# Kernel optimization log

Measured on AMD Instinct MI355X. Metric: run time of the kernel, lower is better.

## Reference

```python
import jax, jax.numpy as jnp
import numpy as np

N = 262144            # inflated nodes (atoms + edge-nodes)
E = 4 * 1024 * 1024   # directed edges
D = 8                 # node_feature_dim
TD = 1                # time_dim
H = 32                # hidden_channels
L = 4                 # num_layers
BN_EPS = 1e-5


def setup_inputs() -> dict:
    key = jax.random.key(0)
    ks = jax.random.split(key, 12)
    s = 0.1  # small init scale
    return {
        "x": jax.random.normal(ks[0], (N, D), jnp.float32),
        "t": jax.random.uniform(ks[1], (1,), jnp.float32),
        "edge_index": jax.random.randint(ks[2], (2, E), 0, N, jnp.int32),
        "node_mask": jax.random.randint(ks[3], (N,), 0, 2) > 0,
        "edge_mask": jax.random.randint(ks[4], (N,), 0, 2) > 0,
        "ond": 5,  # original_node_feature_dim
        "oed": 4,  # original_edge_feature_dim
        # GINConv MLP params: layer 0 has in=D+TD, layers 1..3 have in=H
        "W1_first": jax.random.normal(ks[5], (D + TD, H), jnp.float32) * s,
        "b1_first": jnp.zeros((H,), jnp.float32),
        "W2_first": jax.random.normal(ks[6], (H, H), jnp.float32) * s,
        "b2_first": jnp.zeros((H,), jnp.float32),
        "W1_rest": jax.random.normal(ks[7], (L - 1, H, H), jnp.float32) * s,
        "b1_rest": jnp.zeros((L - 1, H), jnp.float32),
        "W2_rest": jax.random.normal(ks[8], (L - 1, H, H), jnp.float32) * s,
        "b2_rest": jnp.zeros((L - 1, H), jnp.float32),
        "eps": jnp.zeros((L,), jnp.float32),           # train_eps=True, init 0
        "bn_gamma": jnp.ones((L, H), jnp.float32),
        "bn_beta": jnp.zeros((L, H), jnp.float32),
        "lin_W": jax.random.normal(ks[9], (L * H, D), jnp.float32) * s,
        "lin_b": jnp.zeros((D,), jnp.float32),
    }


def _gin_forward(x, t, W1_first, b1_first, W2_first, b2_first,
                 W1_rest, b1_rest, W2_rest, b2_rest, eps, bn_gamma, bn_beta,
                 lin_W, lin_b, edge_index, node_mask, edge_mask, ond, oed):
    src = edge_index[0]
    dst = edge_index[1]
    n = x.shape[0]
    # x_in = cat(x, t*ones)
    tcol = jnp.full((n, 1), t[0], x.dtype)
    h = jnp.concatenate([x, tcol], axis=1)  # [N, D+TD]
    xs = []
    for l in range(L):
        # GINConv: (1+eps)*x_i + sum_{j->i} x_j, then 2-layer MLP
        agg = jax.ops.segment_sum(h[src], dst, num_segments=n)  # scatter-add
        z = (1.0 + eps[l]) * h + agg
        W1 = W1_first if l == 0 else W1_rest[l - 1]
        b1 = b1_first if l == 0 else b1_rest[l - 1]
        W2 = W2_first if l == 0 else W2_rest[l - 1]
        b2 = b2_first if l == 0 else b2_rest[l - 1]
        z = jax.nn.relu(z @ W1 + b1) @ W2 + b2  # [N, H]
        # BatchNorm (training-mode batch stats), then ReLU; dropout=eval->id
        mu = jnp.mean(z, axis=0)
        var = jnp.var(z, axis=0)
        z = (z - mu) * jax.lax.rsqrt(var + BN_EPS) * bn_gamma[l] + bn_beta[l]
        h = jax.nn.relu(z)
        xs.append(h)
    # JK 'cat' + final Linear(L*H -> D)
    new_x = jnp.concatenate(xs, axis=1) @ lin_W + lin_b  # [N, D]
    # masked feature write-back: x[mask, 1:dim+1] = new_x[mask, 1:dim+1]
    cols = jnp.arange(x.shape[1])
    ncols = (cols >= 1) & (cols < ond + 1)
    ecols = (cols >= 1) & (cols < oed + 1)
    out = jnp.where(node_mask[:, None] & ncols[None, :], new_x, x)
    out = jnp.where(edge_mask[:, None] & ecols[None, :], new_x, out)
    return out


def reference(x, t, edge_index, node_mask, edge_mask, ond, oed,
              W1_first, b1_first, W2_first, b2_first,
              W1_rest, b1_rest, W2_rest, b2_rest,
              eps, bn_gamma, bn_beta, lin_W, lin_b):
    return _gin_forward(x, t, W1_first, b1_first, W2_first, b2_first,
                        W1_rest, b1_rest, W2_rest, b2_rest,
                        eps, bn_gamma, bn_beta, lin_W, lin_b,
                        edge_index, node_mask, edge_mask, ond, oed)
```

## Files before the change

kernel.cpp:

```cpp
#include <hip/hip_runtime.h>
#include <cstdint>

#define NN 262144
#define EE 4194304
#define CAP 64
#define NB 512
#define BSZ 512
#define NSH 8
#define SCAP 1280
#define EPB 8192
#define SLICES 64

__device__ inline float bf2f(unsigned short u) {
  union { unsigned int i; float f; } v; v.i = ((unsigned int)u) << 16; return v.f;
}
__device__ inline unsigned short f2bf(float f) {
  union { float f; unsigned int i; } v; v.f = f;
  unsigned int r = v.i + 0x7FFF + ((v.i >> 16) & 1);
  return (unsigned short)(r >> 16);
}
__device__ inline float blo(unsigned int u) {
  union { unsigned int i; float f; } v; v.i = u << 16; return v.f;
}
__device__ inline float bhi(unsigned int u) {
  union { unsigned int i; float f; } v; v.i = u & 0xFFFF0000u; return v.f;
}

__global__ void k_curinit(int* __restrict__ cur) {
  int i = blockIdx.x * 256 + threadIdx.x;
  if (i < NSH * NB) cur[i] = i * SCAP;
}

__global__ void __launch_bounds__(256, 1)
k_bin(const int* __restrict__ ei, int* __restrict__ cur, int* __restrict__ pair) {
  __shared__ int hist[NB];
  __shared__ int off[NB];
  __shared__ int gbase[NB];
  __shared__ int psum[256];
  __shared__ int ebuf[EPB];
  const int tid = threadIdx.x, blk = blockIdx.x, sh = blk & (NSH - 1);
  const int* esrc = ei + (size_t)blk * EPB;
  const int* edst = ei + EE + (size_t)blk * EPB;

  for (int k = tid; k < NB; k += 256) hist[k] = 0;
  __syncthreads();
  for (int j = tid; j < EPB / 4; j += 256) {
    int4 d4 = ((const int4*)edst)[j];
    atomicAdd(&hist[d4.x >> 9], 1);
    atomicAdd(&hist[d4.y >> 9], 1);
    atomicAdd(&hist[d4.z >> 9], 1);
    atomicAdd(&hist[d4.w >> 9], 1);
  }
  __syncthreads();
  int a0 = hist[2 * tid], a1 = hist[2 * tid + 1];
  int ps = a0 + a1;
  psum[tid] = ps;
  __syncthreads();
  for (int d = 1; d < 256; d <<= 1) {
    int v = (tid >= d) ? psum[tid - d] : 0;
    __syncthreads();
    psum[tid] += v;
    __syncthreads();
  }
  int excl = psum[tid] - ps;
  off[2 * tid] = excl;
  off[2 * tid + 1] = excl + a0;
  __syncthreads();
  for (int b = tid; b < NB; b += 256) {
    int n = hist[b];
    int ci = sh * NB + b;
    gbase[b] = n ? atomicAdd(&cur[ci], n) : ci * SCAP;
  }
  __syncthreads();
  for (int k = tid; k < NB; k += 256) hist[k] = off[k];
  __syncthreads();
  for (int j = tid; j < EPB / 4; j += 256) {
    int4 s4 = ((const int4*)esrc)[j];
    int4 d4 = ((const int4*)edst)[j];
    int dd[4] = {d4.x, d4.y, d4.z, d4.w};
    int ss[4] = {s4.x, s4.y, s4.z, s4.w};
#pragma unroll
    for (int u = 0; u < 4; ++u) {
      int bin = dd[u] >> 9, dl = dd[u] & (BSZ - 1);
      int p = atomicAdd(&hist[bin], 1);
      ebuf[p] = ss[u] | (dl << 18);
    }
  }
  __syncthreads();
  for (int b = tid; b < NB; b += 256) {
    int st = off[b];
    int n = hist[b] - st;
    int ci = sh * NB + b;
    int gb = gbase[b];
    int lim = ci * SCAP + SCAP;
    if (gb + n > lim) n = (lim > gb) ? (lim - gb) : 0;
    for (int k = 0; k < n; ++k) pair[gb + k] = ebuf[st + k];
  }
}

__global__ void k_expand(const int* __restrict__ cur, const int* __restrict__ pair,
                         int* __restrict__ slot, int* __restrict__ deg) {
  __shared__ int cbin[BSZ];
  int tid = threadIdx.x;
  int bin = blockIdx.x;
  for (int k = tid; k < BSZ; k += 512) cbin[k] = 0;
  __syncthreads();
  for (int s = 0; s < NSH; ++s) {
    int ci = s * NB + bin, base = ci * SCAP;
    int cnt = min(cur[ci] - base, SCAP);
    for (int k = tid; k < cnt; k += 512) {
      int p = pair[base + k];
      int src = p & 0x3FFFF, dl = p >> 18;
      int pos = atomicAdd(&cbin[dl], 1);
      if (pos < CAP)
        slot[((size_t)bin * BSZ + dl) * CAP + pos] = src;
    }
  }
  __syncthreads();
  for (int k = tid; k < BSZ; k += 512) {
    int cnt = min(cbin[k], CAP);
    int cntp = (cnt + 15) & ~15;
    int self = bin * BSZ + k;
    for (int p = cnt; p < cntp; ++p)
      slot[((size_t)bin * BSZ + k) * CAP + p] = self;
    deg[bin * BSZ + k] = cnt;
  }
}

__global__ void k_layer0(const float* __restrict__ x, const float* __restrict__ t,
                         const int* __restrict__ slot, const int* __restrict__ deg,
                         const float* __restrict__ W1, const float* __restrict__ b1,
                         const float* __restrict__ W2, const float* __restrict__ b2,
                         const float* __restrict__ epsv,
                         unsigned short* __restrict__ zb,
                         float* __restrict__ ssum, float* __restrict__ ssq) {
  __shared__ float W1s[9 * 32];
  __shared__ float W2s[32 * 32];
  __shared__ float aggs[8][8];
  __shared__ float ins[8][12];
  __shared__ float z1s[8][36];
  __shared__ float sqs[8][36];
  int tid = threadIdx.x;
  int c = tid & 31, g = tid >> 5;
  size_t i = (size_t)blockIdx.x * 8 + g;

  for (int k = tid; k < 9 * 32 / 4; k += 256) ((float4*)W1s)[k] = ((const float4*)W1)[k];
  for (int k = tid; k < 32 * 32 / 4; k += 256) ((float4*)W2s)[k] = ((const float4*)W2)[k];

  int cnt = deg[i];
  int cntp = (cnt + 15) & ~15;
  const int* sl = slot + i * CAP;
  int sv = sl[c];
  float t0 = t[0];
  float epsl = epsv[0];
  float xself = (c < 8) ? x[i * 8 + c] : 0.f;

  int q = c & 1, e = c >> 1;
  float4 agg4 = {0.f, 0.f, 0.f, 0.f};
  int kmax = min(cntp, 32);
  for (int k = 0; k < kmax; k += 16) {
    int s = __shfl(sv, k + e, 32);
    float4 v = ((const float4*)x)[(size_t)s * 2 + q];
    agg4.x += v.x; agg4.y += v.y; agg4.z += v.z; agg4.w += v.w;
  }
  if (cntp > 32) {
    int sv2 = sl[32 + c];
    for (int k = 32; k < cntp; k += 16) {
      int s = __shfl(sv2, (k - 32) + e, 32);
      float4 v = ((const float4*)x)[(size_t)s * 2 + q];
      agg4.x += v.x; agg4.y += v.y; agg4.z += v.z; agg4.w += v.w;
    }
  }
#pragma unroll
  for (int off = 2; off < 32; off <<= 1) {
    agg4.x += __shfl_xor(agg4.x, off, 32);
    agg4.y += __shfl_xor(agg4.y, off, 32);
    agg4.z += __shfl_xor(agg4.z, off, 32);
    agg4.w += __shfl_xor(agg4.w, off, 32);
  }
  if (c < 2) ((float4*)aggs[g])[q] = agg4;
  __syncthreads();

  float pad = (float)(cntp - cnt);
  if (c < 8)       ins[g][c] = (1.f + epsl) * xself + aggs[g][c] - pad * xself;
  else if (c == 8) ins[g][8] = (1.f + epsl) * t0 + (float)cnt * t0;
  __syncthreads();

  float acc = b1[c];
#pragma unroll
  for (int d = 0; d < 9; ++d) acc += ins[g][d] * W1s[d * 32 + c];
  float z1 = fmaxf(acc, 0.f);
  z1s[g][c] = z1;
  __syncthreads();

  float acc2 = b2[c];
#pragma unroll
  for (int d = 0; d < 32; ++d) acc2 += z1s[g][d] * W2s[d * 32 + c];
  zb[i * 32 + c] = f2bf(acc2);

  __syncthreads();
  z1s[g][c] = acc2;
  sqs[g][c] = acc2 * acc2;
  __syncthreads();
  if (g == 0) {
    float s1 = 0.f, s2 = 0.f;
#pragma unroll
    for (int n = 0; n < 8; ++n) { s1 += z1s[n][c]; s2 += sqs[n][c]; }
    int slice = blockIdx.x & (SLICES - 1);
    atomicAdd(&ssum[slice * 32 + c], s1);
    atomicAdd(&ssq[slice * 32 + c], s2);
  }
}

__global__ void k_bnapply(const unsigned short* __restrict__ zb,
                          const float* __restrict__ ssum, const float* __restrict__ ssq,
                          const float* __restrict__ gamma, const float* __restrict__ beta,
                          const float* __restrict__ linW,
                          unsigned short* __restrict__ hb,
                          float* __restrict__ out_acc, int first_acc) {
  __shared__ float linWs[256];
  __shared__ float scs[32], shs[32];
  int tid = threadIdx.x;
  for (int k = tid; k < 256; k += 256) linWs[k] = linW[k];
  if (tid < 32) {
    float s1 = 0.f, s2 = 0.f;
    for (int s = 0; s < SLICES; ++s) { s1 += ssum[s * 32 + tid]; s2 += ssq[s * 32 + tid]; }
    float mu = s1 * (1.f / NN);
    float var = s2 * (1.f / NN) - mu * mu;
    float sc = gamma[tid] * rsqrtf(var + 1e-5f);
    scs[tid] = sc;
    shs[tid] = beta[tid] - mu * sc;
  }
  int r = tid & 3;
  size_t n = (size_t)blockIdx.x * 64 + (tid >> 2);
  uint4 u = ((const uint4*)zb)[n * 4 + r];
  __syncthreads();

  float h[8];
#pragma unroll
  for (int j = 0; j < 8; ++j) {
    unsigned int w = (j < 2) ? u.x : (j < 4) ? u.y : (j < 6) ? u.z : u.w;
    float zv = (j & 1) ? bhi(w) : blo(w);
    h[j] = fmaxf(zv * scs[8 * r + j] + shs[8 * r + j], 0.f);
  }
  uint4 o;
  o.x = (unsigned int)f2bf(h[0]) | ((unsigned int)f2bf(h[1]) << 16);
  o.y = (unsigned int)f2bf(h[2]) | ((unsigned int)f2bf(h[3]) << 16);
  o.z = (unsigned int)f2bf(h[4]) | ((unsigned int)f2bf(h[5]) << 16);
  o.w = (unsigned int)f2bf(h[6]) | ((unsigned int)f2bf(h[7]) << 16);
  ((uint4*)hb)[n * 4 + r] = o;

  float jk[8];
#pragma unroll
  for (int d = 0; d < 8; ++d) {
    float a = 0.f;
#pragma unroll
    for (int j = 0; j < 8; ++j) a += h[j] * linWs[(8 * r + j) * 8 + d];
    jk[d] = a;
  }
#pragma unroll
  for (int off = 1; off <= 2; off <<= 1)
#pragma unroll
    for (int d = 0; d < 8; ++d) jk[d] += __shfl_xor(jk[d], off, 64);
  if (r == 0) {
    float4 a0 = {jk[0], jk[1], jk[2], jk[3]};
    float4 a1 = {jk[4], jk[5], jk[6], jk[7]};
    if (!first_acc) {
      float4 p0 = ((const float4*)out_acc)[n * 2];
      float4 p1 = ((const float4*)out_acc)[n * 2 + 1];
      a0.x += p0.x; a0.y += p0.y; a0.z += p0.z; a0.w += p0.w;
      a1.x += p1.x; a1.y += p1.y; a1.z += p1.z; a1.w += p1.w;
    }
    ((float4*)out_acc)[n * 2] = a0;
    ((float4*)out_acc)[n * 2 + 1] = a1;
  }
}

__global__ void k_layerN(const unsigned short* __restrict__ hb,
                         const int* __restrict__ slot, const int* __restrict__ deg,
                         const float* __restrict__ W1, const float* __restrict__ b1,
                         const float* __restrict__ W2, const float* __restrict__ b2,
                         const float* __restrict__ epsv, int l,
                         unsigned short* __restrict__ zbo,
                         float* __restrict__ ssum, float* __restrict__ ssq) {
  __shared__ float W1s[32 * 32];
  __shared__ float W2s[32 * 32];
  __shared__ float aggs[8][32];
  __shared__ float ins[8][36];
  __shared__ float z1s[8][36];
  int tid = threadIdx.x;
  int c = tid & 31, g = tid >> 5;
  size_t i = (size_t)blockIdx.x * 8 + g;

  for (int k = tid; k < 32 * 32 / 4; k += 256) {
    ((float4*)W1s)[k] = ((const float4*)W1)[k];
    ((float4*)W2s)[k] = ((const float4*)W2)[k];
  }

  float epsl = epsv[l];
  int cnt = deg[i];
  int cntp = (cnt + 15) & ~15;
  const int* sl = slot + i * CAP;
  int sv = sl[c];
  float hself = bf2f(hb[i * 32 + c]);

  int q = c & 7, sub = c >> 3;
  const ushort4* h4 = (const ushort4*)hb;
  float4 agg4 = {0.f, 0.f, 0.f, 0.f};
  int kmax = min(cntp, 32);
  for (int k = 0; k < kmax; k += 16) {
    int sa = __shfl(sv, k + sub, 32);
    int sb = __shfl(sv, k + 4 + sub, 32);
    int sc_ = __shfl(sv, k + 8 + sub, 32);
    int sd = __shfl(sv, k + 12 + sub, 32);
    ushort4 ua = h4[(size_t)sa * 8 + q];
    ushort4 ub = h4[(size_t)sb * 8 + q];
    ushort4 uc = h4[(size_t)sc_ * 8 + q];
    ushort4 ud = h4[(size_t)sd * 8 + q];
    agg4.x += bf2f(ua.x) + bf2f(ub.x) + bf2f(uc.x) + bf2f(ud.x);
    agg4.y += bf2f(ua.y) + bf2f(ub.y) + bf2f(uc.y) + bf2f(ud.y);
    agg4.z += bf2f(ua.z) + bf2f(ub.z) + bf2f(uc.z) + bf2f(ud.z);
    agg4.w += bf2f(ua.w) + bf2f(ub.w) + bf2f(uc.w) + bf2f(ud.w);
  }
  if (cntp > 32) {
    int sv2 = sl[32 + c];
    for (int k = 32; k < cntp; k += 16) {
      int kk = k - 32;
      int sa = __shfl(sv2, kk + sub, 32);
      int sb = __shfl(sv2, kk + 4 + sub, 32);
      int sc_ = __shfl(sv2, kk + 8 + sub, 32);
      int sd = __shfl(sv2, kk + 12 + sub, 32);
      ushort4 ua = h4[(size_t)sa * 8 + q];
      ushort4 ub = h4[(size_t)sb * 8 + q];
      ushort4 uc = h4[(size_t)sc_ * 8 + q];
      ushort4 ud = h4[(size_t)sd * 8 + q];
      agg4.x += bf2f(ua.x) + bf2f(ub.x) + bf2f(uc.x) + bf2f(ud.x);
      agg4.y += bf2f(ua.y) + bf2f(ub.y) + bf2f(uc.y) + bf2f(ud.y);
      agg4.z += bf2f(ua.z) + bf2f(ub.z) + bf2f(uc.z) + bf2f(ud.z);
      agg4.w += bf2f(ua.w) + bf2f(ub.w) + bf2f(uc.w) + bf2f(ud.w);
    }
  }
  agg4.x += __shfl_xor(agg4.x, 8, 32);
  agg4.y += __shfl_xor(agg4.y, 8, 32);
  agg4.z += __shfl_xor(agg4.z, 8, 32);
  agg4.w += __shfl_xor(agg4.w, 8, 32);
  agg4.x += __shfl_xor(agg4.x, 16, 32);
  agg4.y += __shfl_xor(agg4.y, 16, 32);
  agg4.z += __shfl_xor(agg4.z, 16, 32);
  agg4.w += __shfl_xor(agg4.w, 16, 32);
  if (c < 8) ((float4*)aggs[g])[q] = agg4;
  __syncthreads();

  float pad = (float)(cntp - cnt);
  float inval = (1.f + epsl - pad) * hself + aggs[g][c];
  ins[g][c] = inval;
  __syncthreads();

  float acc = b1[c];
#pragma unroll
  for (int d = 0; d < 32; ++d) acc += ins[g][d] * W1s[d * 32 + c];
  float z1 = fmaxf(acc, 0.f);
  z1s[g][c] = z1;
  __syncthreads();

  float acc2 = b2[c];
#pragma unroll
  for (int d = 0; d < 32; ++d) acc2 += z1s[g][d] * W2s[d * 32 + c];
  zbo[i * 32 + c] = f2bf(acc2);

  __syncthreads();
  ins[g][c] = acc2;
  z1s[g][c] = acc2 * acc2;
  __syncthreads();
  if (g == 0) {
    float s1 = 0.f, s2 = 0.f;
#pragma unroll
    for (int n = 0; n < 8; ++n) { s1 += ins[n][c]; s2 += z1s[n][c]; }
    int slice = blockIdx.x & (SLICES - 1);
    atomicAdd(&ssum[slice * 32 + c], s1);
    atomicAdd(&ssq[slice * 32 + c], s2);
  }
}

__global__ void k_final(const unsigned short* __restrict__ z3,
                        const float* __restrict__ ssum, const float* __restrict__ ssq,
                        const float* __restrict__ gamma, const float* __restrict__ beta,
                        const float* __restrict__ linW3, const float* __restrict__ lin_b,
                        const float* __restrict__ out_acc, const float* __restrict__ x,
                        const int* __restrict__ nm, const int* __restrict__ em,
                        const int* __restrict__ ondp, const int* __restrict__ oedp,
                        float* __restrict__ out) {
  __shared__ float linWs[256];
  __shared__ float scs[32], shs[32];
  int tid = threadIdx.x;
  for (int k = tid; k < 256; k += 256) linWs[k] = linW3[k];
  if (tid < 32) {
    float s1 = 0.f, s2 = 0.f;
    for (int s = 0; s < SLICES; ++s) { s1 += ssum[s * 32 + tid]; s2 += ssq[s * 32 + tid]; }
    float mu = s1 * (1.f / NN);
    float var = s2 * (1.f / NN) - mu * mu;
    float sc = gamma[tid] * rsqrtf(var + 1e-5f);
    scs[tid] = sc;
    shs[tid] = beta[tid] - mu * sc;
  }
  int r = tid & 3;
  size_t n = (size_t)blockIdx.x * 64 + (tid >> 2);
  uint4 u = ((const uint4*)z3)[n * 4 + r];
  __syncthreads();

  float h[8];
#pragma unroll
  for (int j = 0; j < 8; ++j) {
    unsigned int w = (j < 2) ? u.x : (j < 4) ? u.y : (j < 6) ? u.z : u.w;
    float zv = (j & 1) ? bhi(w) : blo(w);
    h[j] = fmaxf(zv * scs[8 * r + j] + shs[8 * r + j], 0.f);
  }
  float jk[8];
#pragma unroll
  for (int d = 0; d < 8; ++d) {
    float a = 0.f;
#pragma unroll
    for (int j = 0; j < 8; ++j) a += h[j] * linWs[(8 * r + j) * 8 + d];
    jk[d] = a;
  }
#pragma unroll
  for (int off = 1; off <= 2; off <<= 1)
#pragma unroll
    for (int d = 0; d < 8; ++d) jk[d] += __shfl_xor(jk[d], off, 64);
  if (r == 0) {
    float4 p0 = ((const float4*)out_acc)[n * 2];
    float4 p1 = ((const float4*)out_acc)[n * 2 + 1];
    float4 x0 = ((const float4*)x)[n * 2];
    float4 x1 = ((const float4*)x)[n * 2 + 1];
    float res[8] = {jk[0] + p0.x + lin_b[0], jk[1] + p0.y + lin_b[1],
                    jk[2] + p0.z + lin_b[2], jk[3] + p0.w + lin_b[3],
                    jk[4] + p1.x + lin_b[4], jk[5] + p1.y + lin_b[5],
                    jk[6] + p1.z + lin_b[6], jk[7] + p1.w + lin_b[7]};
    float xs[8] = {x0.x, x0.y, x0.z, x0.w, x1.x, x1.y, x1.z, x1.w};
    int ond = ondp[0], oed = oedp[0];
    bool nmv = nm[n] != 0, emv = em[n] != 0;
    float o[8];
#pragma unroll
    for (int d = 0; d < 8; ++d) {
      bool w = (d >= 1) && ((nmv && d < ond + 1) || (emv && d < oed + 1));
      o[d] = w ? res[d] : xs[d];
    }
    ((float4*)out)[n * 2]     = make_float4(o[0], o[1], o[2], o[3]);
    ((float4*)out)[n * 2 + 1] = make_float4(o[4], o[5], o[6], o[7]);
  }
}

extern "C" void kernel_launch(void* const* d_in, const int* in_sizes, int n_in,
                              void* d_out, int out_size, void* d_ws, size_t ws_size,
                              hipStream_t stream) {
  const float* x        = (const float*)d_in[0];
  const float* t        = (const float*)d_in[1];
  const int*   ei       = (const int*)d_in[2];
  const int*   node_mask= (const int*)d_in[3];
  const int*   edge_mask= (const int*)d_in[4];
  const int*   ondp     = (const int*)d_in[5];
  const int*   oedp     = (const int*)d_in[6];
  const float* W1_first = (const float*)d_in[7];
  const float* b1_first = (const float*)d_in[8];
  const float* W2_first = (const float*)d_in[9];
  const float* b2_first = (const float*)d_in[10];
  const float* W1_rest  = (const float*)d_in[11];
  const float* b1_rest  = (const float*)d_in[12];
  const float* W2_rest  = (const float*)d_in[13];
  const float* b2_rest  = (const float*)d_in[14];
  const float* epsv     = (const float*)d_in[15];
  const float* bn_gamma = (const float*)d_in[16];
  const float* bn_beta  = (const float*)d_in[17];
  const float* lin_W    = (const float*)d_in[18];
  const float* lin_b    = (const float*)d_in[19];
  float* out = (float*)d_out;

  char* ws = (char*)d_ws;
  size_t off = 0;
  int*   slot    = (int*)(ws + off);   off += (size_t)NN * CAP * 4;
  int*   pair    = (int*)(ws + off);   off += (size_t)NSH * NB * SCAP * 4;
  int*   cur     = (int*)(ws + off);   off += (size_t)NSH * NB * 4;
  int*   deg     = (int*)(ws + off);   off += (size_t)NN * 4;
  unsigned short* zb = (unsigned short*)(ws + off); off += (size_t)NN * 32 * 2;
  unsigned short* hb = (unsigned short*)(ws + off); off += (size_t)NN * 32 * 2;
  float* out_acc = (float*)(ws + off); off += (size_t)NN * 8 * 4;
  float* stats   = (float*)(ws + off); off += (size_t)4 * 2 * SLICES * 32 * 4;
  (void)ws_size; (void)in_sizes; (void)n_in; (void)out_size;

  hipMemsetAsync(stats, 0, (size_t)4 * 2 * SLICES * 32 * 4, stream);
  k_curinit<<<(NSH * NB + 255) / 256, 256, 0, stream>>>(cur);
  k_bin<<<EE / EPB, 256, 0, stream>>>(ei, cur, pair);
  k_expand<<<NB, 512, 0, stream>>>(cur, pair, slot, deg);

  {
    float* ssum = stats;
    float* ssq  = ssum + SLICES * 32;
    k_layer0<<<NN / 8, 256, 0, stream>>>(x, t, slot, deg, W1_first, b1_first,
                                         W2_first, b2_first, epsv, zb, ssum, ssq);
    k_bnapply<<<NN / 64, 256, 0, stream>>>(zb, ssum, ssq, bn_gamma, bn_beta,
                                           lin_W, hb, out_acc, 1);
  }
  for (int l = 1; l < 4; ++l) {
    const float* W1 = W1_rest + (size_t)(l - 1) * 32 * 32;
    const float* b1 = b1_rest + (size_t)(l - 1) * 32;
    const float* W2 = W2_rest + (size_t)(l - 1) * 32 * 32;
    const float* b2 = b2_rest + (size_t)(l - 1) * 32;
    float* ssum = stats + (size_t)l * 2 * SLICES * 32;
    float* ssq  = ssum + SLICES * 32;
    k_layerN<<<NN / 8, 256, 0, stream>>>(hb, slot, deg, W1, b1, W2, b2,
                                         epsv, l, zb, ssum, ssq);
    if (l < 3)
      k_bnapply<<<NN / 64, 256, 0, stream>>>(zb, ssum, ssq, bn_gamma + l * 32,
                                             bn_beta + l * 32,
                                             lin_W + (size_t)l * 32 * 8,
                                             hb, out_acc, 0);
  }
  k_final<<<NN / 64, 256, 0, stream>>>(zb, stats + 3 * 2 * SLICES * 32,
                                       stats + 3 * 2 * SLICES * 32 + SLICES * 32,
                                       bn_gamma + 96, bn_beta + 96,
                                       lin_W + 3 * 32 * 8, lin_b, out_acc, x,
                                       node_mask, edge_mask, ondp, oedp, out);
}
```

Measured before the change: 578.6 us.

## Compute GIN MLP with split-bf16 MFMA over 16-node tiles

```diff
diff --git a/kernel.cpp b/kernel.cpp
--- a/kernel.cpp
+++ b/kernel.cpp
@@ -10,6 +10,10 @@
 #define SCAP 1280
 #define EPB 8192
 #define SLICES 64
+
+typedef __attribute__((ext_vector_type(8))) short bf16x8;
+typedef __attribute__((ext_vector_type(4))) float f32x4;
+#define MFMA16 __builtin_amdgcn_mfma_f32_16x16x32_bf16
 
 __device__ inline float bf2f(unsigned short u) {
   union { unsigned int i; float f; } v; v.i = ((unsigned int)u) << 16; return v.f;
@@ -134,81 +138,138 @@
                          const float* __restrict__ epsv,
                          unsigned short* __restrict__ zb,
                          float* __restrict__ ssum, float* __restrict__ ssq) {
-  __shared__ float W1s[9 * 32];
-  __shared__ float W2s[32 * 32];
+  __shared__ __align__(16) unsigned short wt1h[32 * 40], wt1l[32 * 40];
+  __shared__ __align__(16) unsigned short wt2h[32 * 40], wt2l[32 * 40];
+  __shared__ __align__(16) unsigned short insh[16 * 40], insl[16 * 40];
+  __shared__ __align__(16) unsigned short z1h[16 * 40], z1l[16 * 40];
   __shared__ float aggs[8][8];
-  __shared__ float ins[8][12];
-  __shared__ float z1s[8][36];
-  __shared__ float sqs[8][36];
   int tid = threadIdx.x;
   int c = tid & 31, g = tid >> 5;
-  size_t i = (size_t)blockIdx.x * 8 + g;
-
-  for (int k = tid; k < 9 * 32 / 4; k += 256) ((float4*)W1s)[k] = ((const float4*)W1)[k];
-  for (int k = tid; k < 32 * 32 / 4; k += 256) ((float4*)W2s)[k] = ((const float4*)W2)[k];
-
-  int cnt = deg[i];
-  int cntp = (cnt + 15) & ~15;
-  const int* sl = slot + i * CAP;
-  int sv = sl[c];
+  size_t base = (size_t)blockIdx.x * 16;
+
+  for (int k = tid; k < 32 * 40; k += 256) { wt1h[k] = 0; wt1l[k] = 0; }
+  for (int k = tid; k < 16 * 40; k += 256) { insh[k] = 0; insl[k] = 0; }
+  __syncthreads();
+  if (tid < 72) {
+    float4 wv = ((const float4*)W1)[tid];
+    int k = tid >> 3, n4 = (tid & 7) * 4;
+    float v[4] = {wv.x, wv.y, wv.z, wv.w};
+#pragma unroll
+    for (int j = 0; j < 4; ++j) {
+      unsigned short h = f2bf(v[j]);
+      wt1h[(n4 + j) * 40 + k] = h;
+      wt1l[(n4 + j) * 40 + k] = f2bf(v[j] - bf2f(h));
+    }
+  }
+  {
+    float4 wv = ((const float4*)W2)[tid];
+    int k = tid >> 3, n4 = (tid & 7) * 4;
+    float v[4] = {wv.x, wv.y, wv.z, wv.w};
+#pragma unroll
+    for (int j = 0; j < 4; ++j) {
+      unsigned short h = f2bf(v[j]);
+      wt2h[(n4 + j) * 40 + k] = h;
+      wt2l[(n4 + j) * 40 + k] = f2bf(v[j] - bf2f(h));
+    }
+  }
+
   float t0 = t[0];
   float epsl = epsv[0];
-  float xself = (c < 8) ? x[i * 8 + c] : 0.f;
-
-  int q = c & 1, e = c >> 1;
-  float4 agg4 = {0.f, 0.f, 0.f, 0.f};
-  int kmax = min(cntp, 32);
-  for (int k = 0; k < kmax; k += 16) {
-    int s = __shfl(sv, k + e, 32);
-    float4 v = ((const float4*)x)[(size_t)s * 2 + q];
-    agg4.x += v.x; agg4.y += v.y; agg4.z += v.z; agg4.w += v.w;
-  }
-  if (cntp > 32) {
-    int sv2 = sl[32 + c];
-    for (int k = 32; k < cntp; k += 16) {
-      int s = __shfl(sv2, (k - 32) + e, 32);
+
+  for (int half = 0; half < 2; ++half) {
+    int row = g + 8 * half;
+    size_t i = base + row;
+    int cnt = deg[i];
+    int cntp = (cnt + 15) & ~15;
+    const int* sl = slot + i * CAP;
+    int sv = sl[c];
+    float xself = (c < 8) ? x[i * 8 + c] : 0.f;
+
+    int q = c & 1, e = c >> 1;
+    float4 agg4 = {0.f, 0.f, 0.f, 0.f};
+    int kmax = min(cntp, 32);
+    for (int k = 0; k < kmax; k += 16) {
+      int s = __shfl(sv, k + e, 32);
       float4 v = ((const float4*)x)[(size_t)s * 2 + q];
       agg4.x += v.x; agg4.y += v.y; agg4.z += v.z; agg4.w += v.w;
     }
-  }
-#pragma unroll
-  for (int off = 2; off < 32; off <<= 1) {
-    agg4.x += __shfl_xor(agg4.x, off, 32);
-    agg4.y += __shfl_xor(agg4.y, off, 32);
-    agg4.z += __shfl_xor(agg4.z, off, 32);
-    agg4.w += __shfl_xor(agg4.w, off, 32);
-  }
-  if (c < 2) ((float4*)aggs[g])[q] = agg4;
-  __syncthreads();
-
-  float pad = (float)(cntp - cnt);
-  if (c < 8)       ins[g][c] = (1.f + epsl) * xself + aggs[g][c] - pad * xself;
-  else if (c == 8) ins[g][8] = (1.f + epsl) * t0 + (float)cnt * t0;
-  __syncthreads();
-
-  float acc = b1[c];
-#pragma unroll
-  for (int d = 0; d < 9; ++d) acc += ins[g][d] * W1s[d * 32 + c];
-  float z1 = fmaxf(acc, 0.f);
-  z1s[g][c] = z1;
-  __syncthreads();
-
-  float acc2 = b2[c];
-#pragma unroll
-  for (int d = 0; d < 32; ++d) acc2 += z1s[g][d] * W2s[d * 32 + c];
-  zb[i * 32 + c] = f2bf(acc2);
-
-  __syncthreads();
-  z1s[g][c] = acc2;
-  sqs[g][c] = acc2 * acc2;
-  __syncthreads();
-  if (g == 0) {
+    if (cntp > 32) {
+      int sv2 = sl[32 + c];
+      for (int k = 32; k < cntp; k += 16) {
+        int s = __shfl(sv2, (k - 32) + e, 32);
+        float4 v = ((const float4*)x)[(size_t)s * 2 + q];
+        agg4.x += v.x; agg4.y += v.y; agg4.z += v.z; agg4.w += v.w;
+      }
+    }
+#pragma unroll
+    for (int off = 2; off < 32; off <<= 1) {
+      agg4.x += __shfl_xor(agg4.x, off, 32);
+      agg4.y += __shfl_xor(agg4.y, off, 32);
+      agg4.z += __shfl_xor(agg4.z, off, 32);
+      agg4.w += __shfl_xor(agg4.w, off, 32);
+    }
+    if (c < 2) ((float4*)aggs[g])[q] = agg4;
+    __syncthreads();
+
+    float pad = (float)(cntp - cnt);
+    if (c < 9) {
+      float inval = (c < 8) ? ((1.f + epsl) * xself + aggs[g][c] - pad * xself)
+                            : ((1.f + epsl) * t0 + (float)cnt * t0);
+      unsigned short h = f2bf(inval);
+      insh[row * 40 + c] = h;
+      insl[row * 40 + c] = f2bf(inval - bf2f(h));
+    }
+    __syncthreads();
+  }
+
+  int w = tid >> 6, lane = tid & 63;
+  int nsel = (w & 1) * 16 + (lane & 15);
+  int kb = (lane >> 4) * 8;
+  if (w < 2) {
+    bf16x8 ah = *(const bf16x8*)&insh[(lane & 15) * 40 + kb];
+    bf16x8 al = *(const bf16x8*)&insl[(lane & 15) * 40 + kb];
+    bf16x8 bh = *(const bf16x8*)&wt1h[nsel * 40 + kb];
+    bf16x8 bl = *(const bf16x8*)&wt1l[nsel * 40 + kb];
+    f32x4 c1 = {0.f, 0.f, 0.f, 0.f};
+    c1 = MFMA16(ah, bh, c1, 0, 0, 0);
+    c1 = MFMA16(al, bh, c1, 0, 0, 0);
+    c1 = MFMA16(ah, bl, c1, 0, 0, 0);
+    float bias1 = b1[nsel];
+#pragma unroll
+    for (int r = 0; r < 4; ++r) {
+      int rr = (lane >> 4) * 4 + r;
+      float z = fmaxf(c1[r] + bias1, 0.f);
+      unsigned short h = f2bf(z);
+      z1h[rr * 40 + nsel] = h;
+      z1l[rr * 40 + nsel] = f2bf(z - bf2f(h));
+    }
+  }
+  __syncthreads();
+  if (w < 2) {
+    bf16x8 ah = *(const bf16x8*)&z1h[(lane & 15) * 40 + kb];
+    bf16x8 al = *(const bf16x8*)&z1l[(lane & 15) * 40 + kb];
+    bf16x8 bh = *(const bf16x8*)&wt2h[nsel * 40 + kb];
+    bf16x8 bl = *(const bf16x8*)&wt2l[nsel * 40 + kb];
+    f32x4 c2 = {0.f, 0.f, 0.f, 0.f};
+    c2 = MFMA16(ah, bh, c2, 0, 0, 0);
+    c2 = MFMA16(al, bh, c2, 0, 0, 0);
+    c2 = MFMA16(ah, bl, c2, 0, 0, 0);
+    float bias2 = b2[nsel];
     float s1 = 0.f, s2 = 0.f;
 #pragma unroll
-    for (int n = 0; n < 8; ++n) { s1 += z1s[n][c]; s2 += sqs[n][c]; }
-    int slice = blockIdx.x & (SLICES - 1);
-    atomicAdd(&ssum[slice * 32 + c], s1);
-    atomicAdd(&ssq[slice * 32 + c], s2);
+    for (int r = 0; r < 4; ++r) {
+      int rr = (lane >> 4) * 4 + r;
+      float z = c2[r] + bias2;
+      zb[(base + rr) * 32 + nsel] = f2bf(z);
+      s1 += z; s2 += z * z;
+    }
+    s1 += __shfl_xor(s1, 16, 64); s2 += __shfl_xor(s2, 16, 64);
+    s1 += __shfl_xor(s1, 32, 64); s2 += __shfl_xor(s2, 32, 64);
+    if ((lane >> 4) == 0) {
+      int slice = blockIdx.x & (SLICES - 1);
+      atomicAdd(&ssum[slice * 32 + nsel], s1);
+      atomicAdd(&ssq[slice * 32 + nsel], s2);
+    }
   }
 }
 
@@ -283,53 +344,52 @@
                          const float* __restrict__ epsv, int l,
                          unsigned short* __restrict__ zbo,
                          float* __restrict__ ssum, float* __restrict__ ssq) {
-  __shared__ float W1s[32 * 32];
-  __shared__ float W2s[32 * 32];
+  __shared__ __align__(16) unsigned short wt1h[32 * 40], wt1l[32 * 40];
+  __shared__ __align__(16) unsigned short wt2h[32 * 40], wt2l[32 * 40];
+  __shared__ __align__(16) unsigned short insh[16 * 40], insl[16 * 40];
+  __shared__ __align__(16) unsigned short z1h[16 * 40], z1l[16 * 40];
   __shared__ float aggs[8][32];
-  __shared__ float ins[8][36];
-  __shared__ float z1s[8][36];
   int tid = threadIdx.x;
   int c = tid & 31, g = tid >> 5;
-  size_t i = (size_t)blockIdx.x * 8 + g;
-
-  for (int k = tid; k < 32 * 32 / 4; k += 256) {
-    ((float4*)W1s)[k] = ((const float4*)W1)[k];
-    ((float4*)W2s)[k] = ((const float4*)W2)[k];
+  size_t base = (size_t)blockIdx.x * 16;
+
+  {
+    float4 w1v = ((const float4*)W1)[tid];
+    float4 w2v = ((const float4*)W2)[tid];
+    int k = tid >> 3, n4 = (tid & 7) * 4;
+    float v1[4] = {w1v.x, w1v.y, w1v.z, w1v.w};
+    float v2[4] = {w2v.x, w2v.y, w2v.z, w2v.w};
+#pragma unroll
+    for (int j = 0; j < 4; ++j) {
+      unsigned short h1 = f2bf(v1[j]);
+      wt1h[(n4 + j) * 40 + k] = h1;
+      wt1l[(n4 + j) * 40 + k] = f2bf(v1[j] - bf2f(h1));
+      unsigned short h2 = f2bf(v2[j]);
+      wt2h[(n4 + j) * 40 + k] = h2;
+      wt2l[(n4 + j) * 40 + k] = f2bf(v2[j] - bf2f(h2));
+    }
   }
 
   float epsl = epsv[l];
-  int cnt = deg[i];
-  int cntp = (cnt + 15) & ~15;
-  const int* sl = slot + i * CAP;
-  int sv = sl[c];
-  float hself = bf2f(hb[i * 32 + c]);
-
-  int q = c & 7, sub = c >> 3;
-  const ushort4* h4 = (const ushort4*)hb;
-  float4 agg4 = {0.f, 0.f, 0.f, 0.f};
-  int kmax = min(cntp, 32);
-  for (int k = 0; k < kmax; k += 16) {
-    int sa = __shfl(sv, k + sub, 32);
-    int sb = __shfl(sv, k + 4 + sub, 32);
-    int sc_ = __shfl(sv, k + 8 + sub, 32);
-    int sd = __shfl(sv, k + 12 + sub, 32);
-    ushort4 ua = h4[(size_t)sa * 8 + q];
-    ushort4 ub = h4[(size_t)sb * 8 + q];
-    ushort4 uc = h4[(size_t)sc_ * 8 + q];
-    ushort4 ud = h4[(size_t)sd * 8 + q];
-    agg4.x += bf2f(ua.x) + bf2f(ub.x) + bf2f(uc.x) + bf2f(ud.x);
-    agg4.y += bf2f(ua.y) + bf2f(ub.y) + bf2f(uc.y) + bf2f(ud.y);
-    agg4.z += bf2f(ua.z) + bf2f(ub.z) + bf2f(uc.z) + bf2f(ud.z);
-    agg4.w += bf2f(ua.w) + bf2f(ub.w) + bf2f(uc.w) + bf2f(ud.w);
-  }
-  if (cntp > 32) {
-    int sv2 = sl[32 + c];
-    for (int k = 32; k < cntp; k += 16) {
-      int kk = k - 32;
-      int sa = __shfl(sv2, kk + sub, 32);
-      int sb = __shfl(sv2, kk + 4 + sub, 32);
-      int sc_ = __shfl(sv2, kk + 8 + sub, 32);
-      int sd = __shfl(sv2, kk + 12 + sub, 32);
+
+  for (int half = 0; half < 2; ++half) {
+    int row = g + 8 * half;
+    size_t i = base + row;
+    int cnt = deg[i];
+    int cntp = (cnt + 15) & ~15;
+    const int* sl = slot + i * CAP;
+    int sv = sl[c];
+    float hself = bf2f(hb[i * 32 + c]);
+
+    int q = c & 7, sub = c >> 3;
+    const ushort4* h4 = (const ushort4*)hb;
+    float4 agg4 = {0.f, 0.f, 0.f, 0.f};
+    int kmax = min(cntp, 32);
+    for (int k = 0; k < kmax; k += 16) {
+      int sa = __shfl(sv, k + sub, 32);
+      int sb = __shfl(sv, k + 4 + sub, 32);
+      int sc_ = __shfl(sv, k + 8 + sub, 32);
+      int sd = __shfl(sv, k + 12 + sub, 32);
       ushort4 ua = h4[(size_t)sa * 8 + q];
       ushort4 ub = h4[(size_t)sb * 8 + q];
       ushort4 uc = h4[(size_t)sc_ * 8 + q];
@@ -339,46 +399,91 @@
       agg4.z += bf2f(ua.z) + bf2f(ub.z) + bf2f(uc.z) + bf2f(ud.z);
       agg4.w += bf2f(ua.w) + bf2f(ub.w) + bf2f(uc.w) + bf2f(ud.w);
     }
-  }
-  agg4.x += __shfl_xor(agg4.x, 8, 32);
-  agg4.y += __shfl_xor(agg4.y, 8, 32);
-  agg4.z += __shfl_xor(agg4.z, 8, 32);
-  agg4.w += __shfl_xor(agg4.w, 8, 32);
-  agg4.x += __shfl_xor(agg4.x, 16, 32);
-  agg4.y += __shfl_xor(agg4.y, 16, 32);
-  agg4.z += __shfl_xor(agg4.z, 16, 32);
-  agg4.w += __shfl_xor(agg4.w, 16, 32);
-  if (c < 8) ((float4*)aggs[g])[q] = agg4;
-  __syncthreads();
-
-  float pad = (float)(cntp - cnt);
-  float inval = (1.f + epsl - pad) * hself + aggs[g][c];
-  ins[g][c] = inval;
-  __syncthreads();
-
-  float acc = b1[c];
-#pragma unroll
-  for (int d = 0; d < 32; ++d) acc += ins[g][d] * W1s[d * 32 + c];
-  float z1 = fmaxf(acc, 0.f);
-  z1s[g][c] = z1;
-  __syncthreads();
-
-  float acc2 = b2[c];
-#pragma unroll
-  for (int d = 0; d < 32; ++d) acc2 += z1s[g][d] * W2s[d * 32 + c];
-  zbo[i * 32 + c] = f2bf(acc2);
-
-  __syncthreads();
-  ins[g][c] = acc2;
-  z1s[g][c] = acc2 * acc2;
-  __syncthreads();
-  if (g == 0) {
+    if (cntp > 32) {
+      int sv2 = sl[32 + c];
+      for (int k = 32; k < cntp; k += 16) {
+        int kk = k - 32;
+        int sa = __shfl(sv2, kk + sub, 32);
+        int sb = __shfl(sv2, kk + 4 + sub, 32);
+        int sc_ = __shfl(sv2, kk + 8 + sub, 32);
+        int sd = __shfl(sv2, kk + 12 + sub, 32);
+        ushort4 ua = h4[(size_t)sa * 8 + q];
+        ushort4 ub = h4[(size_t)sb * 8 + q];
+        ushort4 uc = h4[(size_t)sc_ * 8 + q];
+        ushort4 ud = h4[(size_t)sd * 8 + q];
+        agg4.x += bf2f(ua.x) + bf2f(ub.x) + bf2f(uc.x) + bf2f(ud.x);
+        agg4.y += bf2f(ua.y) + bf2f(ub.y) + bf2f(uc.y) + bf2f(ud.y);
+        agg4.z += bf2f(ua.z) + bf2f(ub.z) + bf2f(uc.z) + bf2f(ud.z);
+        agg4.w += bf2f(ua.w) + bf2f(ub.w) + bf2f(uc.w) + bf2f(ud.w);
+      }
+    }
+    agg4.x += __shfl_xor(agg4.x, 8, 32);
+    agg4.y += __shfl_xor(agg4.y, 8, 32);
+    agg4.z += __shfl_xor(agg4.z, 8, 32);
+    agg4.w += __shfl_xor(agg4.w, 8, 32);
+    agg4.x += __shfl_xor(agg4.x, 16, 32);
+    agg4.y += __shfl_xor(agg4.y, 16, 32);
+    agg4.z += __shfl_xor(agg4.z, 16, 32);
+    agg4.w += __shfl_xor(agg4.w, 16, 32);
+    if (c < 8) ((float4*)aggs[g])[q] = agg4;
+    __syncthreads();
+
+    float pad = (float)(cntp - cnt);
+    float inval = (1.f + epsl - pad) * hself + aggs[g][c];
+    unsigned short h = f2bf(inval);
+    insh[row * 40 + c] = h;
+    insl[row * 40 + c] = f2bf(inval - bf2f(h));
+    __syncthreads();
+  }
+
+  int w = tid >> 6, lane = tid & 63;
+  int nsel = (w & 1) * 16 + (lane & 15);
+  int kb = (lane >> 4) * 8;
+  if (w < 2) {
+    bf16x8 ah = *(const bf16x8*)&insh[(lane & 15) * 40 + kb];
+    bf16x8 al = *(const bf16x8*)&insl[(lane & 15) * 40 + kb];
+    bf16x8 bh = *(const bf16x8*)&wt1h[nsel * 40 + kb];
+    bf16x8 bl = *(const bf16x8*)&wt1l[nsel * 40 + kb];
+    f32x4 c1 = {0.f, 0.f, 0.f, 0.f};
+    c1 = MFMA16(ah, bh, c1, 0, 0, 0);
+    c1 = MFMA16(al, bh, c1, 0, 0, 0);
+    c1 = MFMA16(ah, bl, c1, 0, 0, 0);
+    float bias1 = b1[nsel];
+#pragma unroll
+    for (int r = 0; r < 4; ++r) {
+      int rr = (lane >> 4) * 4 + r;
+      float z = fmaxf(c1[r] + bias1, 0.f);
+      unsigned short h = f2bf(z);
+      z1h[rr * 40 + nsel] = h;
+      z1l[rr * 40 + nsel] = f2bf(z - bf2f(h));
+    }
+  }
+  __syncthreads();
+  if (w < 2) {
+    bf16x8 ah = *(const bf16x8*)&z1h[(lane & 15) * 40 + kb];
+    bf16x8 al = *(const bf16x8*)&z1l[(lane & 15) * 40 + kb];
+    bf16x8 bh = *(const bf16x8*)&wt2h[nsel * 40 + kb];
+    bf16x8 bl = *(const bf16x8*)&wt2l[nsel * 40 + kb];
+    f32x4 c2 = {0.f, 0.f, 0.f, 0.f};
+    c2 = MFMA16(ah, bh, c2, 0, 0, 0);
+    c2 = MFMA16(al, bh, c2, 0, 0, 0);
+    c2 = MFMA16(ah, bl, c2, 0, 0, 0);
+    float bias2 = b2[nsel];
     float s1 = 0.f, s2 = 0.f;
 #pragma unroll
-    for (int n = 0; n < 8; ++n) { s1 += ins[n][c]; s2 += z1s[n][c]; }
-    int slice = blockIdx.x & (SLICES - 1);
-    atomicAdd(&ssum[slice * 32 + c], s1);
-    atomicAdd(&ssq[slice * 32 + c], s2);
+    for (int r = 0; r < 4; ++r) {
+      int rr = (lane >> 4) * 4 + r;
+      float z = c2[r] + bias2;
+      zbo[(base + rr) * 32 + nsel] = f2bf(z);
+      s1 += z; s2 += z * z;
+    }
+    s1 += __shfl_xor(s1, 16, 64); s2 += __shfl_xor(s2, 16, 64);
+    s1 += __shfl_xor(s1, 32, 64); s2 += __shfl_xor(s2, 32, 64);
+    if ((lane >> 4) == 0) {
+      int slice = blockIdx.x & (SLICES - 1);
+      atomicAdd(&ssum[slice * 32 + nsel], s1);
+      atomicAdd(&ssq[slice * 32 + nsel], s2);
+    }
   }
 }
 
@@ -495,8 +600,8 @@
   {
     float* ssum = stats;
     float* ssq  = ssum + SLICES * 32;
-    k_layer0<<<NN / 8, 256, 0, stream>>>(x, t, slot, deg, W1_first, b1_first,
-                                         W2_first, b2_first, epsv, zb, ssum, ssq);
+    k_layer0<<<NN / 16, 256, 0, stream>>>(x, t, slot, deg, W1_first, b1_first,
+                                          W2_first, b2_first, epsv, zb, ssum, ssq);
     k_bnapply<<<NN / 64, 256, 0, stream>>>(zb, ssum, ssq, bn_gamma, bn_beta,
                                            lin_W, hb, out_acc, 1);
   }
@@ -507,8 +612,8 @@
     const float* b2 = b2_rest + (size_t)(l - 1) * 32;
     float* ssum = stats + (size_t)l * 2 * SLICES * 32;
     float* ssq  = ssum + SLICES * 32;
-    k_layerN<<<NN / 8, 256, 0, stream>>>(hb, slot, deg, W1, b1, W2, b2,
-                                         epsv, l, zb, ssum, ssq);
+    k_layerN<<<NN / 16, 256, 0, stream>>>(hb, slot, deg, W1, b1, W2, b2,
+                                          epsv, l, zb, ssum, ssq);
     if (l < 3)
       k_bnapply<<<NN / 64, 256, 0, stream>>>(zb, ssum, ssq, bn_gamma + l * 32,
                                              bn_beta + l * 32,
```

Measured after the change: 523.0 us. -9.6%, faster.
